# Performance work log

Measured on AMD Instinct MI355X. Metric: run time of the kernel, lower is better.

## Reference

```python
import jax, jax.numpy as jnp
import numpy as np

E, D_MODEL, D_FF = 8, 1024, 4096
B, S = 4, 2048


def setup_inputs() -> dict:
    key = jax.random.key(0)
    ks = jax.random.split(key, 7)
    scale_in = 1.0 / np.sqrt(D_MODEL)
    scale_ff = 1.0 / np.sqrt(D_FF)
    return {
        "x": jax.random.normal(ks[0], (B, S, D_MODEL), dtype=jnp.float32),
        "w1": jax.random.normal(ks[1], (E, D_MODEL, D_FF), dtype=jnp.float32) * scale_in,
        "b1": jax.random.normal(ks[2], (E, D_FF), dtype=jnp.float32) * 0.01,
        "w2": jax.random.normal(ks[3], (E, D_FF, D_MODEL), dtype=jnp.float32) * scale_ff,
        "b2": jax.random.normal(ks[4], (E, D_MODEL), dtype=jnp.float32) * 0.01,
        "gate_w": jax.random.normal(ks[5], (D_MODEL, E), dtype=jnp.float32) * scale_in,
        "gate_b": jax.random.normal(ks[6], (E,), dtype=jnp.float32) * 0.01,
    }


def reference(x, w1, b1, w2, b2, gate_w, gate_b):
    # Gating: softmax then top-1 (argmax of probs == argmax of logits)
    gate_logits = x @ gate_w + gate_b                      # [B,S,E]
    gate_probs = jax.nn.softmax(gate_logits, axis=-1)
    top1 = jnp.argmax(gate_probs, axis=-1)                 # [B,S] int
    mask = jax.nn.one_hot(top1, E, dtype=x.dtype)          # [B,S,E]

    # Dense compute of every expert on every token (faithful to source)
    h = jax.nn.relu(jnp.einsum('bsd,edf->ebsf', x, w1) + b1[:, None, None, :])  # [E,B,S,F]
    y = jnp.einsum('ebsf,efd->ebsd', h, w2) + b2[:, None, None, :]              # [E,B,S,D]

    # Top-1 mask-and-sum combine (note: no gate-prob scaling in the original)
    out = jnp.einsum('ebsd,bse->bsd', y, mask)             # [B,S,D]
    return out
```

## Files before the change

kernel.cpp:

```cpp
#include <hip/hip_runtime.h>
#include <stdint.h>

#define DM 1024
#define DF 4096
#define NE 8
#define NTOK 8192
#define MT_LAUNCH 72

typedef __attribute__((ext_vector_type(8))) short short8;
typedef __attribute__((ext_vector_type(8))) unsigned short ushort8v;
typedef __attribute__((ext_vector_type(4))) float floatx4;

__device__ inline unsigned short f2bf(float f) {
    union { float f; unsigned u; } v; v.f = f;
    unsigned u = v.u;
    u += 0x7fffu + ((u >> 16) & 1u);
    return (unsigned short)(u >> 16);
}

#define GLDS(g, l) __builtin_amdgcn_global_load_lds( \
    (const __attribute__((address_space(1))) void*)(g), \
    (__attribute__((address_space(3))) void*)(l), 16, 0, 0)

__global__ void gate_kernel(const float* __restrict__ x, const float* __restrict__ gw,
                            const float* __restrict__ gb, int* __restrict__ top1,
                            unsigned short* __restrict__ xb) {
    int t = blockIdx.x;
    int lane = threadIdx.x;
    const float* xr = x + (size_t)t * DM;
    unsigned short* xbr = xb + (size_t)t * DM;
    double acc[NE];
#pragma unroll
    for (int e = 0; e < NE; ++e) acc[e] = 0.0;
    for (int j = 0; j < DM / 64; ++j) {
        int d = j * 64 + lane;
        float xf = xr[d];
        xbr[d] = f2bf(xf);
        double xv = (double)xf;
        const float* g = gw + (size_t)d * NE;
#pragma unroll
        for (int e = 0; e < NE; ++e) acc[e] = fma(xv, (double)g[e], acc[e]);
    }
#pragma unroll
    for (int e = 0; e < NE; ++e) {
        for (int off = 32; off > 0; off >>= 1)
            acc[e] += __shfl_down(acc[e], off, 64);
    }
    if (lane == 0) {
        int best = 0;
        double bv = acc[0] + (double)gb[0];
        for (int e = 1; e < NE; ++e) {
            double v = acc[e] + (double)gb[e];
            if (v > bv) { bv = v; best = e; }
        }
        top1[t] = best;
    }
}

__global__ void count_kernel(const int* __restrict__ top1, int* __restrict__ ctrl) {
    int t = blockIdx.x * 256 + threadIdx.x;
    int e = top1[t];
    int lane = threadIdx.x & 63;
#pragma unroll
    for (int ex = 0; ex < NE; ++ex) {
        unsigned long long m = __ballot(e == ex);
        if (m != 0ull && lane == (__ffsll((long long)m) - 1))
            atomicAdd(&ctrl[ex], __popcll(m));
    }
}

__global__ void prefix_kernel(int* ctrl) {
    if (threadIdx.x == 0) {
        int s = 0, t = 0;
        for (int e = 0; e < NE; ++e) {
            int cnt = ctrl[e];
            ctrl[8 + e] = s; ctrl[17 + e] = s;
            for (int m = 0; m * 128 < cnt; ++m) {
                ctrl[32 + 3 * t] = e;
                ctrl[33 + 3 * t] = s + m * 128;
                int rr = cnt - m * 128;
                ctrl[34 + 3 * t] = rr < 128 ? rr : 128;
                ++t;
            }
            s += cnt;
        }
        ctrl[16] = s;
        ctrl[25] = t;
    }
}

__global__ void scatter_kernel(const int* __restrict__ top1, int* __restrict__ ctrl,
                               int* __restrict__ perm) {
    int t = blockIdx.x * 256 + threadIdx.x;
    int e = top1[t];
    int lane = threadIdx.x & 63;
#pragma unroll
    for (int ex = 0; ex < NE; ++ex) {
        unsigned long long m = __ballot(e == ex);
        if (m == 0ull) continue;
        int leader = __ffsll((long long)m) - 1;
        int base = 0;
        if (lane == leader) base = atomicAdd(&ctrl[17 + ex], __popcll(m));
        base = __shfl(base, leader, 64);
        if (e == ex) {
            int pos = __popcll(m & ((1ull << lane) - 1ull));
            perm[base + pos] = t;
        }
    }
}

__global__ void transpose_bf16(const float* __restrict__ src, unsigned short* __restrict__ dst,
                               int R, int C) {
    __shared__ float tile[64][65];
    int tilesR = R >> 6, tilesC = C >> 6;
    int bid = blockIdx.x;
    int e = bid / (tilesR * tilesC);
    int rem = bid % (tilesR * tilesC);
    int tr = rem / tilesC, tc = rem % tilesC;
    const float* s = src + (size_t)e * R * C + (size_t)(tr * 64) * C + tc * 64;
    unsigned short* d = dst + (size_t)e * R * C + (size_t)(tc * 64) * R + tr * 64;
    int tid = threadIdx.x;
#pragma unroll
    for (int i = 0; i < 4; ++i) {
        int idx = i * 256 + tid;
        int r = idx >> 4, c4 = (idx & 15) * 4;
        float4 v = *(const float4*)(s + (size_t)r * C + c4);
        tile[r][c4 + 0] = v.x; tile[r][c4 + 1] = v.y;
        tile[r][c4 + 2] = v.z; tile[r][c4 + 3] = v.w;
    }
    __syncthreads();
#pragma unroll
    for (int i = 0; i < 2; ++i) {
        int idx = i * 256 + tid;
        int c = idx >> 3, r8 = (idx & 7) * 8;
        ushort8v o;
#pragma unroll
        for (int j = 0; j < 8; ++j) o[j] = f2bf(tile[r8 + j][c]);
        *(ushort8v*)(d + (size_t)c * R + r8) = o;
    }
}

#define STAGE(BUF, KK) do { \
    _Pragma("unroll") \
    for (int i_ = 0; i_ < 4; ++i_) { \
        GLDS(arow[i_] + (KK), &As[BUF][(i_ * 256 + tid) * 8]); \
        GLDS(brow[i_] + (KK), &Bs[BUF][(i_ * 256 + tid) * 8]); \
    } } while (0)

#define COMPUTE(BUF) do { \
    _Pragma("unroll") \
    for (int ks_ = 0; ks_ < 2; ++ks_) { \
        short8 af[4], bfr[4]; \
        _Pragma("unroll") \
        for (int m_ = 0; m_ < 4; ++m_) { \
            int R_ = wm + m_ * 16 + (lane & 15); \
            int s_ = (ks_ * 4 + (lane >> 4)) ^ (R_ & 7); \
            af[m_] = *(const short8*)&As[BUF][R_ * 64 + s_ * 8]; \
        } \
        _Pragma("unroll") \
        for (int n_ = 0; n_ < 4; ++n_) { \
            int R_ = wn + n_ * 16 + (lane & 15); \
            int s_ = (ks_ * 4 + (lane >> 4)) ^ (R_ & 7); \
            bfr[n_] = *(const short8*)&Bs[BUF][R_ * 64 + s_ * 8]; \
        } \
        _Pragma("unroll") \
        for (int m_ = 0; m_ < 4; ++m_) \
            _Pragma("unroll") \
            for (int n_ = 0; n_ < 4; ++n_) \
                acc[m_][n_] = __builtin_amdgcn_mfma_f32_16x16x32_bf16(af[m_], bfr[n_], acc[m_][n_], 0, 0, 0); \
    } } while (0)

template<bool FFN1>
__global__ __launch_bounds__(256) void ffn_gemm(
    const unsigned short* __restrict__ A,
    const unsigned short* __restrict__ Bt,
    const float* __restrict__ bias,
    const int* __restrict__ ctrl,
    const int* __restrict__ perm,
    unsigned short* __restrict__ Hout,
    float* __restrict__ Yout) {
    constexpr int K  = FFN1 ? DM : DF;
    constexpr int N  = FFN1 ? DF : DM;
    constexpr int KS = FFN1 ? 1 : 2;
    constexpr int KLEN = K / KS;
    constexpr int NT = N / 128;
    constexpr int G = 8;
    constexpr int INNER = NT * KS;
    constexpr int NKI = KLEN / 64;

    int nwg = gridDim.x;
    int bo = blockIdx.x;
    int q = nwg >> 3, r = nwg & 7;
    int xcd = bo & 7, lid = bo >> 3;
    int b = (xcd < r ? xcd * (q + 1) : r * (q + 1) + (xcd - r) * q) + lid;

    int grp = b / (G * INNER);
    int ii = b % (G * INNER);
    int nt  = ii / (G * KS);
    int rem = ii % (G * KS);
    int til = grp * G + rem / KS;
    int ksp = rem % KS;
    if (til >= ctrl[25]) return;
    int e       = ctrl[32 + 3 * til];
    int rowbase = ctrl[33 + 3 * til];
    int rows    = ctrl[34 + 3 * til];

    __shared__ __align__(16) unsigned short As[2][128 * 64];
    __shared__ __align__(16) unsigned short Bs[2][128 * 64];

    int tid = threadIdx.x;
    int lane = tid & 63;
    int wave = tid >> 6;
    int wm = (wave & 1) * 64;
    int wn = (wave >> 1) * 64;

    const unsigned short* arow[4];
    const unsigned short* brow[4];
    const unsigned short* bbase = Bt + (size_t)e * N * K + (size_t)(nt * 128) * K;
#pragma unroll
    for (int i = 0; i < 4; ++i) {
        int c = i * 256 + tid;
        int rr2 = c >> 3;
        int gk = (c & 7) ^ (rr2 & 7);
        int rr = rr2 < rows ? rr2 : rows - 1;
        int cr = rowbase + rr;
        int srow = FFN1 ? perm[cr] : cr;
        arow[i] = A + (size_t)srow * K + gk * 8;
        brow[i] = bbase + (size_t)rr2 * K + gk * 8;
    }

    floatx4 acc[4][4];
#pragma unroll
    for (int i = 0; i < 4; ++i)
#pragma unroll
        for (int j = 0; j < 4; ++j) acc[i][j] = floatx4{0.f, 0.f, 0.f, 0.f};

    int kk0 = ksp * KLEN;

    STAGE(0, kk0);
    __syncthreads();
#pragma unroll 1
    for (int t = 0; t < NKI; t += 2) {
        int kk = kk0 + t * 64;
        STAGE(1, kk + 64);
        COMPUTE(0);
        __syncthreads();
        if (t + 2 < NKI) STAGE(0, kk + 128);
        COMPUTE(1);
        __syncthreads();
    }

    int col0 = nt * 128 + wn + (lane & 15);
    int rowq = (lane >> 4) * 4;
    float bv[4];
#pragma unroll
    for (int n = 0; n < 4; ++n) bv[n] = (FFN1 || ksp == 0) ? bias[e * N + col0 + n * 16] : 0.f;

#pragma unroll
    for (int m = 0; m < 4; ++m) {
#pragma unroll
        for (int r2 = 0; r2 < 4; ++r2) {
            int lr = wm + m * 16 + rowq + r2;
            if (lr < rows) {
                if (FFN1) {
                    unsigned short* hr = Hout + (size_t)(rowbase + lr) * DF + col0;
#pragma unroll
                    for (int n = 0; n < 4; ++n) {
                        float v = acc[m][n][r2] + bv[n];
                        v = v > 0.f ? v : 0.f;
                        hr[n * 16] = f2bf(v);
                    }
                } else {
                    float* yr = Yout + (size_t)perm[rowbase + lr] * DM + col0;
#pragma unroll
                    for (int n = 0; n < 4; ++n)
                        atomicAdd(&yr[n * 16], acc[m][n][r2] + bv[n]);
                }
            }
        }
    }
}

#undef STAGE
#undef COMPUTE

extern "C" void kernel_launch(void* const* d_in, const int* in_sizes, int n_in,
                              void* d_out, int out_size, void* d_ws, size_t ws_size,
                              hipStream_t stream) {
    const float* x  = (const float*)d_in[0];
    const float* w1 = (const float*)d_in[1];
    const float* b1 = (const float*)d_in[2];
    const float* w2 = (const float*)d_in[3];
    const float* b2 = (const float*)d_in[4];
    const float* gw = (const float*)d_in[5];
    const float* gb = (const float*)d_in[6];
    float* out = (float*)d_out;

    char* ws = (char*)d_ws;
    int* ctrl = (int*)ws;
    int* top1 = (int*)(ws + 1024);
    int* perm = (int*)(ws + 1024 + 32768);
    size_t o = 66560;
    unsigned short* xb  = (unsigned short*)(ws + o);        o += (size_t)NTOK * DM * 2;
    unsigned short* w1t = (unsigned short*)(ws + o);        o += (size_t)NE * DM * DF * 2;
    unsigned short* w2t = (unsigned short*)(ws + o);        o += (size_t)NE * DM * DF * 2;
    unsigned short* H   = (unsigned short*)(ws + o);

    hipMemsetAsync(ctrl, 0, 1024, stream);
    hipMemsetAsync(out, 0, (size_t)out_size * 4, stream);
    gate_kernel<<<NTOK, 64, 0, stream>>>(x, gw, gb, top1, xb);
    count_kernel<<<NTOK / 256, 256, 0, stream>>>(top1, ctrl);
    prefix_kernel<<<1, 64, 0, stream>>>(ctrl);
    scatter_kernel<<<NTOK / 256, 256, 0, stream>>>(top1, ctrl, perm);
    transpose_bf16<<<NE * (DM / 64) * (DF / 64), 256, 0, stream>>>(w1, w1t, DM, DF);
    transpose_bf16<<<NE * (DF / 64) * (DM / 64), 256, 0, stream>>>(w2, w2t, DF, DM);
    ffn_gemm<true ><<<MT_LAUNCH * (DF / 128), 256, 0, stream>>>(xb, w1t, b1, ctrl, perm, H, nullptr);
    ffn_gemm<false><<<MT_LAUNCH * (DM / 128) * 2, 256, 0, stream>>>(H, w2t, b2, ctrl, perm, nullptr, out);
}
```

Baseline: 645.4 us.

## Use 256x256 4-stage pipelined FFN1 GEMM and drop split-K atomics in FFN2

FFN1 becomes its own kernel with 512-thread blocks and 256x256 tiles. It uses a 4-deep LDS ring buffer of 32-wide K slabs, explicit vmcnt waits, sched barriers and setprio around the MFMA bursts, aiming for higher MFMA utilisation and better operand reuse. FFN2 drops the 2-way split-K, writes outputs directly instead of using atomicAdd, and the output memset is removed. The prefix kernel now builds separate 256-row and 128-row tile lists. In exchange FFN2 launches half as many blocks, and the larger FFN1 tiles waste more rows on partial expert tiles.

```diff
diff --git a/kernel.cpp b/kernel.cpp
--- a/kernel.cpp
+++ b/kernel.cpp
@@ -5,7 +5,8 @@
 #define DF 4096
 #define NE 8
 #define NTOK 8192
-#define MT_LAUNCH 72
+#define MT128 72
+#define MT256 40
 
 typedef __attribute__((ext_vector_type(8))) short short8;
 typedef __attribute__((ext_vector_type(8))) unsigned short ushort8v;
@@ -21,6 +22,11 @@
 #define GLDS(g, l) __builtin_amdgcn_global_load_lds( \
     (const __attribute__((address_space(1))) void*)(g), \
     (__attribute__((address_space(3))) void*)(l), 16, 0, 0)
+
+#define VMW(N)  asm volatile("s_waitcnt vmcnt(" #N ")" ::: "memory")
+#define LGKM0   asm volatile("s_waitcnt lgkmcnt(0)" ::: "memory")
+#define SCHED0  __builtin_amdgcn_sched_barrier(0)
+#define BAR     __builtin_amdgcn_s_barrier()
 
 __global__ void gate_kernel(const float* __restrict__ x, const float* __restrict__ gw,
                             const float* __restrict__ gb, int* __restrict__ top1,
@@ -71,21 +77,29 @@
 
 __global__ void prefix_kernel(int* ctrl) {
     if (threadIdx.x == 0) {
-        int s = 0, t = 0;
+        int s = 0, t256 = 0, t128 = 0;
         for (int e = 0; e < NE; ++e) {
             int cnt = ctrl[e];
             ctrl[8 + e] = s; ctrl[17 + e] = s;
+            for (int m = 0; m * 256 < cnt; ++m) {
+                ctrl[32 + 3 * t256] = e;
+                ctrl[33 + 3 * t256] = s + m * 256;
+                int rr = cnt - m * 256;
+                ctrl[34 + 3 * t256] = rr < 256 ? rr : 256;
+                ++t256;
+            }
             for (int m = 0; m * 128 < cnt; ++m) {
-                ctrl[32 + 3 * t] = e;
-                ctrl[33 + 3 * t] = s + m * 128;
+                ctrl[160 + 3 * t128] = e;
+                ctrl[161 + 3 * t128] = s + m * 128;
                 int rr = cnt - m * 128;
-                ctrl[34 + 3 * t] = rr < 128 ? rr : 128;
-                ++t;
+                ctrl[162 + 3 * t128] = rr < 128 ? rr : 128;
+                ++t128;
             }
             s += cnt;
         }
         ctrl[16] = s;
-        ctrl[25] = t;
+        ctrl[25] = t256;
+        ctrl[26] = t128;
     }
 }
 
@@ -140,14 +154,204 @@
     }
 }
 
-#define STAGE(BUF, KK) do { \
+#define F1_SLAB(u, SU, STG, W) do { \
+    if (STG) { \
+        int kk_ = ((SU) + 3) * 32; \
+        GLDS(ap0 + kk_, &As[((u) + 3) & 3][(size_t)tid * 8]); \
+        GLDS(ap1 + kk_, &As[((u) + 3) & 3][(size_t)(512 + tid) * 8]); \
+        GLDS(bp0 + kk_, &Bs[((u) + 3) & 3][(size_t)tid * 8]); \
+        GLDS(bp1 + kk_, &Bs[((u) + 3) & 3][(size_t)(512 + tid) * 8]); \
+    } \
+    short8 af[8], bf[4]; \
+    _Pragma("unroll") \
+    for (int m_ = 0; m_ < 8; ++m_) af[m_] = *(const short8*)&As[u][aoff[m_]]; \
+    _Pragma("unroll") \
+    for (int n_ = 0; n_ < 4; ++n_) bf[n_] = *(const short8*)&Bs[u][boff[n_]]; \
+    LGKM0; SCHED0; \
+    __builtin_amdgcn_s_setprio(1); \
+    _Pragma("unroll") \
+    for (int m_ = 0; m_ < 8; ++m_) \
+        _Pragma("unroll") \
+        for (int n_ = 0; n_ < 4; ++n_) \
+            acc[m_][n_] = __builtin_amdgcn_mfma_f32_16x16x32_bf16(af[m_], bf[n_], acc[m_][n_], 0, 0, 0); \
+    __builtin_amdgcn_s_setprio(0); \
+    W; SCHED0; BAR; \
+} while (0)
+
+__global__ __launch_bounds__(512, 2) void ffn1_gemm(
+    const unsigned short* __restrict__ A,
+    const unsigned short* __restrict__ Bt,
+    const float* __restrict__ bias,
+    const int* __restrict__ ctrl,
+    const int* __restrict__ perm,
+    unsigned short* __restrict__ Hout) {
+    constexpr int K = DM;
+    constexpr int N = DF;
+    constexpr int NT = N / 256;
+    constexpr int NKI = K / 32;
+    constexpr int SLABSZ = 256 * 32;
+    constexpr int G = 8;
+
+    int nwg = gridDim.x;
+    int bo = blockIdx.x;
+    int q = nwg >> 3, r = nwg & 7;
+    int xcd = bo & 7, lid = bo >> 3;
+    int b = (xcd < r ? xcd * (q + 1) : r * (q + 1) + (xcd - r) * q) + lid;
+
+    int grp = b / (G * NT);
+    int ii = b % (G * NT);
+    int nt = ii / G;
+    int til = grp * G + (ii % G);
+    if (til >= ctrl[25]) return;
+    int e       = ctrl[32 + 3 * til];
+    int rowbase = ctrl[33 + 3 * til];
+    int rows    = ctrl[34 + 3 * til];
+
+    __shared__ __align__(16) unsigned short As[4][SLABSZ];
+    __shared__ __align__(16) unsigned short Bs[4][SLABSZ];
+
+    int tid = threadIdx.x, lane = tid & 63, wave = tid >> 6;
+    int wm = (wave >> 2) * 128;
+    int wn = (wave & 3) * 64;
+
+    int rA0 = tid >> 2, rA1 = 128 + (tid >> 2);
+    int kofs = ((tid & 3) ^ ((tid >> 3) & 3)) * 8;
+    int c0 = rowbase + (rA0 < rows ? rA0 : rows - 1);
+    int c1 = rowbase + (rA1 < rows ? rA1 : rows - 1);
+    const unsigned short* ap0 = A + (size_t)perm[c0] * K + kofs;
+    const unsigned short* ap1 = A + (size_t)perm[c1] * K + kofs;
+    const unsigned short* bb  = Bt + (size_t)e * N * K + (size_t)(nt * 256) * K + kofs;
+    const unsigned short* bp0 = bb + (size_t)rA0 * K;
+    const unsigned short* bp1 = bb + (size_t)rA1 * K;
+
+    int aoff[8], boff[4];
+#pragma unroll
+    for (int m = 0; m < 8; ++m) {
+        int R = wm + m * 16 + (lane & 15);
+        aoff[m] = R * 32 + (((lane >> 4) ^ ((R >> 1) & 3)) * 8);
+    }
+#pragma unroll
+    for (int n = 0; n < 4; ++n) {
+        int R = wn + n * 16 + (lane & 15);
+        boff[n] = R * 32 + (((lane >> 4) ^ ((R >> 1) & 3)) * 8);
+    }
+
+    floatx4 acc[8][4];
+#pragma unroll
+    for (int i = 0; i < 8; ++i)
+#pragma unroll
+        for (int j = 0; j < 4; ++j) acc[i][j] = floatx4{0.f, 0.f, 0.f, 0.f};
+
+#pragma unroll
+    for (int s = 0; s < 3; ++s) {
+        GLDS(ap0 + s * 32, &As[s][(size_t)tid * 8]);
+        GLDS(ap1 + s * 32, &As[s][(size_t)(512 + tid) * 8]);
+        GLDS(bp0 + s * 32, &Bs[s][(size_t)tid * 8]);
+        GLDS(bp1 + s * 32, &Bs[s][(size_t)(512 + tid) * 8]);
+    }
+    VMW(8); SCHED0; BAR;
+
+#pragma unroll 1
+    for (int s = 0; s < NKI - 4; s += 4) {
+        F1_SLAB(0, s + 0, 1, VMW(8));
+        F1_SLAB(1, s + 1, 1, VMW(8));
+        F1_SLAB(2, s + 2, 1, VMW(8));
+        F1_SLAB(3, s + 3, 1, VMW(8));
+    }
+    F1_SLAB(0, NKI - 4, 1, VMW(8));
+    F1_SLAB(1, NKI - 3, 0, VMW(4));
+    F1_SLAB(2, NKI - 2, 0, VMW(0));
+    F1_SLAB(3, NKI - 1, 0, (void)0);
+
+    int col0 = nt * 256 + wn + (lane & 15);
+    int rowq = (lane >> 4) * 4;
+    float bv[4];
+#pragma unroll
+    for (int n = 0; n < 4; ++n) bv[n] = bias[e * N + col0 + n * 16];
+
+#pragma unroll
+    for (int m = 0; m < 8; ++m) {
+#pragma unroll
+        for (int r2 = 0; r2 < 4; ++r2) {
+            int lr = wm + m * 16 + rowq + r2;
+            if (lr < rows) {
+                unsigned short* hr = Hout + (size_t)(rowbase + lr) * DF + col0;
+#pragma unroll
+                for (int n = 0; n < 4; ++n) {
+                    float v = acc[m][n][r2] + bv[n];
+                    v = v > 0.f ? v : 0.f;
+                    hr[n * 16] = f2bf(v);
+                }
+            }
+        }
+    }
+}
+#undef F1_SLAB
+
+__global__ __launch_bounds__(256) void ffn2_gemm(
+    const unsigned short* __restrict__ A,
+    const unsigned short* __restrict__ Bt,
+    const float* __restrict__ bias,
+    const int* __restrict__ ctrl,
+    const int* __restrict__ perm,
+    float* __restrict__ Yout) {
+    constexpr int K = DF;
+    constexpr int N = DM;
+    constexpr int NT = N / 128;
+    constexpr int G = 8;
+    constexpr int NKI = K / 64;
+
+    int nwg = gridDim.x;
+    int bo = blockIdx.x;
+    int q = nwg >> 3, r = nwg & 7;
+    int xcd = bo & 7, lid = bo >> 3;
+    int b = (xcd < r ? xcd * (q + 1) : r * (q + 1) + (xcd - r) * q) + lid;
+
+    int grp = b / (G * NT);
+    int ii = b % (G * NT);
+    int nt = ii / G;
+    int til = grp * G + (ii % G);
+    if (til >= ctrl[26]) return;
+    int e       = ctrl[160 + 3 * til];
+    int rowbase = ctrl[161 + 3 * til];
+    int rows    = ctrl[162 + 3 * til];
+
+    __shared__ __align__(16) unsigned short As[2][128 * 64];
+    __shared__ __align__(16) unsigned short Bs[2][128 * 64];
+
+    int tid = threadIdx.x;
+    int lane = tid & 63;
+    int wave = tid >> 6;
+    int wm = (wave & 1) * 64;
+    int wn = (wave >> 1) * 64;
+
+    const unsigned short* arow[4];
+    const unsigned short* brow[4];
+    const unsigned short* bbase = Bt + (size_t)e * N * K + (size_t)(nt * 128) * K;
+#pragma unroll
+    for (int i = 0; i < 4; ++i) {
+        int c = i * 256 + tid;
+        int rr2 = c >> 3;
+        int gk = (c & 7) ^ (rr2 & 7);
+        int rr = rr2 < rows ? rr2 : rows - 1;
+        arow[i] = A + (size_t)(rowbase + rr) * K + gk * 8;
+        brow[i] = bbase + (size_t)rr2 * K + gk * 8;
+    }
+
+    floatx4 acc[4][4];
+#pragma unroll
+    for (int i = 0; i < 4; ++i)
+#pragma unroll
+        for (int j = 0; j < 4; ++j) acc[i][j] = floatx4{0.f, 0.f, 0.f, 0.f};
+
+#define F2_STAGE(BUF, KK) do { \
     _Pragma("unroll") \
     for (int i_ = 0; i_ < 4; ++i_) { \
         GLDS(arow[i_] + (KK), &As[BUF][(i_ * 256 + tid) * 8]); \
         GLDS(brow[i_] + (KK), &Bs[BUF][(i_ * 256 + tid) * 8]); \
     } } while (0)
 
-#define COMPUTE(BUF) do { \
+#define F2_COMPUTE(BUF) do { \
     _Pragma("unroll") \
     for (int ks_ = 0; ks_ < 2; ++ks_) { \
         short8 af[4], bfr[4]; \
@@ -170,91 +374,26 @@
                 acc[m_][n_] = __builtin_amdgcn_mfma_f32_16x16x32_bf16(af[m_], bfr[n_], acc[m_][n_], 0, 0, 0); \
     } } while (0)
 
-template<bool FFN1>
-__global__ __launch_bounds__(256) void ffn_gemm(
-    const unsigned short* __restrict__ A,
-    const unsigned short* __restrict__ Bt,
-    const float* __restrict__ bias,
-    const int* __restrict__ ctrl,
-    const int* __restrict__ perm,
-    unsigned short* __restrict__ Hout,
-    float* __restrict__ Yout) {
-    constexpr int K  = FFN1 ? DM : DF;
-    constexpr int N  = FFN1 ? DF : DM;
-    constexpr int KS = FFN1 ? 1 : 2;
-    constexpr int KLEN = K / KS;
-    constexpr int NT = N / 128;
-    constexpr int G = 8;
-    constexpr int INNER = NT * KS;
-    constexpr int NKI = KLEN / 64;
-
-    int nwg = gridDim.x;
-    int bo = blockIdx.x;
-    int q = nwg >> 3, r = nwg & 7;
-    int xcd = bo & 7, lid = bo >> 3;
-    int b = (xcd < r ? xcd * (q + 1) : r * (q + 1) + (xcd - r) * q) + lid;
-
-    int grp = b / (G * INNER);
-    int ii = b % (G * INNER);
-    int nt  = ii / (G * KS);
-    int rem = ii % (G * KS);
-    int til = grp * G + rem / KS;
-    int ksp = rem % KS;
-    if (til >= ctrl[25]) return;
-    int e       = ctrl[32 + 3 * til];
-    int rowbase = ctrl[33 + 3 * til];
-    int rows    = ctrl[34 + 3 * til];
-
-    __shared__ __align__(16) unsigned short As[2][128 * 64];
-    __shared__ __align__(16) unsigned short Bs[2][128 * 64];
-
-    int tid = threadIdx.x;
-    int lane = tid & 63;
-    int wave = tid >> 6;
-    int wm = (wave & 1) * 64;
-    int wn = (wave >> 1) * 64;
-
-    const unsigned short* arow[4];
-    const unsigned short* brow[4];
-    const unsigned short* bbase = Bt + (size_t)e * N * K + (size_t)(nt * 128) * K;
-#pragma unroll
-    for (int i = 0; i < 4; ++i) {
-        int c = i * 256 + tid;
-        int rr2 = c >> 3;
-        int gk = (c & 7) ^ (rr2 & 7);
-        int rr = rr2 < rows ? rr2 : rows - 1;
-        int cr = rowbase + rr;
-        int srow = FFN1 ? perm[cr] : cr;
-        arow[i] = A + (size_t)srow * K + gk * 8;
-        brow[i] = bbase + (size_t)rr2 * K + gk * 8;
-    }
-
-    floatx4 acc[4][4];
-#pragma unroll
-    for (int i = 0; i < 4; ++i)
-#pragma unroll
-        for (int j = 0; j < 4; ++j) acc[i][j] = floatx4{0.f, 0.f, 0.f, 0.f};
-
-    int kk0 = ksp * KLEN;
-
-    STAGE(0, kk0);
+    F2_STAGE(0, 0);
     __syncthreads();
 #pragma unroll 1
     for (int t = 0; t < NKI; t += 2) {
-        int kk = kk0 + t * 64;
-        STAGE(1, kk + 64);
-        COMPUTE(0);
+        int kk = t * 64;
+        F2_STAGE(1, kk + 64);
+        F2_COMPUTE(0);
         __syncthreads();
-        if (t + 2 < NKI) STAGE(0, kk + 128);
-        COMPUTE(1);
+        if (t + 2 < NKI) F2_STAGE(0, kk + 128);
+        F2_COMPUTE(1);
         __syncthreads();
     }
+#undef F2_STAGE
+#undef F2_COMPUTE
 
     int col0 = nt * 128 + wn + (lane & 15);
     int rowq = (lane >> 4) * 4;
     float bv[4];
 #pragma unroll
-    for (int n = 0; n < 4; ++n) bv[n] = (FFN1 || ksp == 0) ? bias[e * N + col0 + n * 16] : 0.f;
+    for (int n = 0; n < 4; ++n) bv[n] = bias[e * N + col0 + n * 16];
 
 #pragma unroll
     for (int m = 0; m < 4; ++m) {
@@ -262,27 +401,14 @@
         for (int r2 = 0; r2 < 4; ++r2) {
             int lr = wm + m * 16 + rowq + r2;
             if (lr < rows) {
-                if (FFN1) {
-                    unsigned short* hr = Hout + (size_t)(rowbase + lr) * DF + col0;
-#pragma unroll
-                    for (int n = 0; n < 4; ++n) {
-                        float v = acc[m][n][r2] + bv[n];
-                        v = v > 0.f ? v : 0.f;
-                        hr[n * 16] = f2bf(v);
-                    }
-                } else {
-                    float* yr = Yout + (size_t)perm[rowbase + lr] * DM + col0;
-#pragma unroll
-                    for (int n = 0; n < 4; ++n)
-                        atomicAdd(&yr[n * 16], acc[m][n][r2] + bv[n]);
-                }
+                float* yr = Yout + (size_t)perm[rowbase + lr] * DM + col0;
+#pragma unroll
+                for (int n = 0; n < 4; ++n)
+                    yr[n * 16] = acc[m][n][r2] + bv[n];
             }
         }
     }
 }
-
-#undef STAGE
-#undef COMPUTE
 
 extern "C" void kernel_launch(void* const* d_in, const int* in_sizes, int n_in,
                               void* d_out, int out_size, void* d_ws, size_t ws_size,
@@ -298,22 +424,21 @@
 
     char* ws = (char*)d_ws;
     int* ctrl = (int*)ws;
-    int* top1 = (int*)(ws + 1024);
-    int* perm = (int*)(ws + 1024 + 32768);
-    size_t o = 66560;
+    int* top1 = (int*)(ws + 2048);
+    int* perm = (int*)(ws + 2048 + 32768);
+    size_t o = 67584;
     unsigned short* xb  = (unsigned short*)(ws + o);        o += (size_t)NTOK * DM * 2;
     unsigned short* w1t = (unsigned short*)(ws + o);        o += (size_t)NE * DM * DF * 2;
     unsigned short* w2t = (unsigned short*)(ws + o);        o += (size_t)NE * DM * DF * 2;
     unsigned short* H   = (unsigned short*)(ws + o);
 
-    hipMemsetAsync(ctrl, 0, 1024, stream);
-    hipMemsetAsync(out, 0, (size_t)out_size * 4, stream);
+    hipMemsetAsync(ctrl, 0, 2048, stream);
     gate_kernel<<<NTOK, 64, 0, stream>>>(x, gw, gb, top1, xb);
     count_kernel<<<NTOK / 256, 256, 0, stream>>>(top1, ctrl);
     prefix_kernel<<<1, 64, 0, stream>>>(ctrl);
     scatter_kernel<<<NTOK / 256, 256, 0, stream>>>(top1, ctrl, perm);
     transpose_bf16<<<NE * (DM / 64) * (DF / 64), 256, 0, stream>>>(w1, w1t, DM, DF);
     transpose_bf16<<<NE * (DF / 64) * (DM / 64), 256, 0, stream>>>(w2, w2t, DF, DM);
-    ffn_gemm<true ><<<MT_LAUNCH * (DF / 128), 256, 0, stream>>>(xb, w1t, b1, ctrl, perm, H, nullptr);
-    ffn_gemm<false><<<MT_LAUNCH * (DM / 128) * 2, 256, 0, stream>>>(H, w2t, b2, ctrl, perm, nullptr, out);
-}
+    ffn1_gemm<<<MT256 * (DF / 256), 512, 0, stream>>>(xb, w1t, b1, ctrl, perm, H);
+    ffn2_gemm<<<MT128 * (DM / 128), 256, 0, stream>>>(H, w2t, b2, ctrl, perm, out);
+}
```

Measured after the change: 625.8 us. -3.0%, faster.
